# Performance work log

Measured on AMD Instinct MI355X. Metric: run time of the kernel, lower is better.

The kernel has to match this reference:

```python
import jax, jax.numpy as jnp
import numpy as np

N_EMBD = 1024
N_HEAD = 16


def setup_inputs() -> dict:
    key = jax.random.key(0)
    ks = jax.random.split(key, 5)
    B, T, C = 2, 2048, N_EMBD
    x = jax.random.normal(ks[0], (B, T, C), dtype=jnp.float32)
    # parameters (stored as (in, out); forward uses x @ W + b, equivalent to torch Linear)
    s1 = 1.0 / np.sqrt(C)
    W_attn = jax.random.normal(ks[1], (C, 3 * C), dtype=jnp.float32) * s1
    b_attn = jnp.zeros((3 * C,), dtype=jnp.float32)
    W_proj = jax.random.normal(ks[2], (C, C), dtype=jnp.float32) * s1
    b_proj = jnp.zeros((C,), dtype=jnp.float32)
    return {"x": x, "W_attn": W_attn, "b_attn": b_attn, "W_proj": W_proj, "b_proj": b_proj}


def reference(x, W_attn, b_attn, W_proj, b_proj):
    B, T, C = x.shape
    H = N_HEAD
    D = C // H  # head dim
    qkv = x @ W_attn + b_attn                       # [B, T, 3C]
    q, k, v = jnp.split(qkv, 3, axis=-1)
    # [B, H, T, D]
    q = q.reshape(B, T, H, D).transpose(0, 2, 1, 3)
    k = k.reshape(B, T, H, D).transpose(0, 2, 1, 3)
    v = v.reshape(B, T, H, D).transpose(0, 2, 1, 3)
    scale = 1.0 / jnp.sqrt(jnp.asarray(D, dtype=q.dtype))
    wei = jnp.einsum("bhqd,bhkd->bhqk", q, k) * scale  # [B, H, T, T]
    causal = jnp.tril(jnp.ones((T, T), dtype=bool))
    wei = jnp.where(causal[None, None, :, :], wei, -jnp.inf)
    wei = jax.nn.softmax(wei, axis=-1)
    y = jnp.einsum("bhqk,bhkd->bhqd", wei, v)          # [B, H, T, D]
    y = y.transpose(0, 2, 1, 3).reshape(B, T, C)
    return y @ W_proj + b_proj
```

## Files before the change

### kernel.cpp

```cpp
#include <hip/hip_runtime.h>
#include <hip/hip_bf16.h>

typedef __attribute__((ext_vector_type(8))) short short8;
typedef __attribute__((ext_vector_type(4))) float floatx4;
typedef __attribute__((ext_vector_type(4))) unsigned int uintx4;
#define BF16 __hip_bfloat16

__device__ __forceinline__ unsigned short f2bf(float f) {
  unsigned int u = __builtin_bit_cast(unsigned int, f);
  unsigned int r = (u + 0x7FFFu + ((u >> 16) & 1u)) >> 16;
  return (unsigned short)r;
}

__device__ __forceinline__ unsigned int cvt_pk_bf16(float lo, float hi) {
  unsigned int r;
  asm("v_cvt_pk_bf16_f32 %0, %1, %2" : "=v"(r) : "v"(lo), "v"(hi));
  return r;
}

__device__ __forceinline__ void gload_lds16(const void* g, void* l) {
  __builtin_amdgcn_global_load_lds(
      (const __attribute__((address_space(1))) unsigned int*)g,
      (__attribute__((address_space(3))) unsigned int*)l, 16, 0, 0);
}

__global__ __launch_bounds__(256)
void cvt_bf16(const float* __restrict__ in, unsigned short* __restrict__ out, int n) {
  int i = (blockIdx.x * 256 + threadIdx.x) * 8;
  if (i >= n) return;
  float4 a = *(const float4*)(in + i);
  float4 b = *(const float4*)(in + i + 4);
  short8 v;
  v[0] = (short)f2bf(a.x); v[1] = (short)f2bf(a.y);
  v[2] = (short)f2bf(a.z); v[3] = (short)f2bf(a.w);
  v[4] = (short)f2bf(b.x); v[5] = (short)f2bf(b.y);
  v[6] = (short)f2bf(b.z); v[7] = (short)f2bf(b.w);
  *(short8*)(out + i) = v;
}

__global__ __launch_bounds__(256)
void transpose_cvt(const float* __restrict__ in, unsigned short* __restrict__ out,
                   int K, int N) {
  __shared__ float tile[64][65];
  const int nb = N >> 6;
  const int tn = blockIdx.x % nb, tk = blockIdx.x / nb;
  const int n0 = tn << 6, k0 = tk << 6;
  const int tid = threadIdx.x;
#pragma unroll
  for (int c = 0; c < 4; ++c) {
    int t = tid + c * 256;
    int r = t >> 4, col = (t & 15) << 2;
    float4 v = *(const float4*)(in + (size_t)(k0 + r) * N + n0 + col);
    tile[r][col] = v.x; tile[r][col + 1] = v.y;
    tile[r][col + 2] = v.z; tile[r][col + 3] = v.w;
  }
  __syncthreads();
#pragma unroll
  for (int c = 0; c < 2; ++c) {
    int t = tid + c * 256;
    int r = t >> 3, col = (t & 7) << 3;
    short8 v;
#pragma unroll
    for (int j = 0; j < 8; ++j) v[j] = (short)f2bf(tile[col + j][r]);
    *(short8*)(out + (size_t)(n0 + r) * K + k0 + col) = v;
  }
}

template <int EPI>
__global__ __launch_bounds__(256, 2)
void gemm_bt(const BF16* __restrict__ A, const BF16* __restrict__ Bt,
             const float* __restrict__ bias, void* __restrict__ outv,
             int M, int N, int K) {
  const int tid = threadIdx.x;
  const int w = tid >> 6, l = tid & 63;
  const int lr = l & 15, lg = l >> 4;
  const int nbx = N >> 7;
  const int bm = blockIdx.x / nbx, bn = blockIdx.x % nbx;
  const int row0 = bm << 7, col0 = bn << 7;
  const int wr = (w >> 1) << 6, wc = (w & 1) << 6;

  __shared__ __align__(16) BF16 ldsA[128 * 64];
  __shared__ __align__(16) BF16 ldsB[128 * 64];

  floatx4 acc[4][4] = {};
  const int swzl = (lr & 7) << 3;

  for (int k0 = 0; k0 < K; k0 += 64) {
#pragma unroll
    for (int c = 0; c < 4; ++c) {
      int t = w * 64 + l + c * 256;
      int ar = t >> 3;
      int ch = (t & 7) ^ (ar & 7);
      gload_lds16(A + (size_t)(row0 + ar) * K + k0 + (ch << 3),
                  ldsA + w * 512 + c * 2048);
      gload_lds16(Bt + (size_t)(col0 + ar) * K + k0 + (ch << 3),
                  ldsB + w * 512 + c * 2048);
    }
    __syncthreads();
#pragma unroll
    for (int kk = 0; kk < 64; kk += 32) {
      short8 af[4], bf[4];
#pragma unroll
      for (int m = 0; m < 4; ++m)
        af[m] = *(const short8*)(ldsA + (wr + m * 16 + lr) * 64 + ((kk + lg * 8) ^ swzl));
#pragma unroll
      for (int n = 0; n < 4; ++n)
        bf[n] = *(const short8*)(ldsB + (wc + n * 16 + lr) * 64 + ((kk + lg * 8) ^ swzl));
#pragma unroll
      for (int m = 0; m < 4; ++m)
#pragma unroll
        for (int n = 0; n < 4; ++n)
          acc[m][n] = __builtin_amdgcn_mfma_f32_16x16x32_bf16(af[m], bf[n], acc[m][n], 0, 0, 0);
    }
    __syncthreads();
  }

#pragma unroll
  for (int m = 0; m < 4; ++m)
#pragma unroll
    for (int n = 0; n < 4; ++n)
#pragma unroll
      for (int j = 0; j < 4; ++j) {
        int row = row0 + wr + m * 16 + lg * 4 + j;
        int col = col0 + wc + n * 16 + lr;
        float v = acc[m][n][j] + bias[col];
        if (EPI == 0) {
          BF16* out = (BF16*)outv;
          int s = col >> 10, cc = col & 1023;
          int hh = cc >> 6, dd = cc & 63;
          int bb = row >> 11, tt = row & 2047;
          size_t addr;
          if (s == 2)
            addr = (size_t)8388608 + (((size_t)bb * 16 + hh) * 64 + dd) * 2048 + tt;
          else
            addr = (size_t)s * 4194304 + (((size_t)bb * 16 + hh) * 2048 + tt) * 64 + dd;
          out[addr] = __float2bfloat16(v);
        } else {
          float* out = (float*)outv;
          out[(size_t)row * N + col] = v;
        }
      }
}

__global__ __launch_bounds__(256, 4)
void flash_attn(const BF16* __restrict__ qkv, BF16* __restrict__ y) {
  const int T = 2048;
  const int i = blockIdx.x;
  const int xcd = i & 7, s = i >> 3;
  const int par = (s ^ (s >> 5)) & 1;
  const int rnk = ((s >> 5) << 4) | ((s & 31) >> 1);
  const int bh = xcd * 4 + (rnk & 3);
  const int hq = rnk >> 2;
  const int qt = par ? hq : (31 - hq);
  const int b = bh >> 4, h = bh & 15;
  const int q0 = qt << 6;
  const int tid = threadIdx.x, w = tid >> 6, l = tid & 63;
  const int lr = l & 15, lg = l >> 4;

  const BF16* Q  = qkv + (size_t)bh * T * 64;
  const BF16* Kp = qkv + 4194304 + (size_t)bh * T * 64;
  const BF16* Vt = qkv + 8388608 + (size_t)bh * 64 * T;

  __shared__ __align__(16) BF16 ldsK[2][4096];
  __shared__ __align__(16) BF16 ldsV[2][6144];

  const float C1 = 0.18033688011112042f;
  const float C2 = 17.312340490667562f;
  const int swzl = (lr & 7) << 3;
  const int nt = qt + 1;

  short8 qf[2];
#pragma unroll
  for (int c = 0; c < 2; ++c)
    qf[c] = *(const short8*)(Q + (size_t)(q0 + w * 16 + lr) * 64 + c * 32 + lg * 8);

  floatx4 acc_o[4] = {};
  floatx4 lsum4 = {0.f, 0.f, 0.f, 0.f};

  const int t0 = w * 64 + l, t1 = t0 + 256;
  const int r0 = t0 >> 3, ch0 = (t0 & 7) ^ (r0 & 7);
  const int r1 = t1 >> 3, ch1 = (t1 & 7) ^ (r1 & 7);
  const BF16* kg0 = Kp + ((size_t)r0 << 6) + ch0 * 8;
  const BF16* kg1 = Kp + ((size_t)r1 << 6) + ch1 * 8;
  const BF16* vg0 = Vt + (size_t)r0 * T + ch0 * 8;
  const BF16* vg1 = Vt + (size_t)r1 * T + ch1 * 8;

#define STAGE2(BUF)                                           \
  {                                                           \
    gload_lds16(kg0, &ldsK[BUF][w * 512]);                    \
    gload_lds16(vg0, &ldsV[BUF][w * 512]);                    \
    gload_lds16(kg1, &ldsK[BUF][w * 512 + 2048]);             \
    gload_lds16(vg1, &ldsV[BUF][w * 512 + 2048]);             \
    kg0 += 4096; kg1 += 4096; vg0 += 64; vg1 += 64;           \
  }

#define TILE(IT, MASKED)                                                      \
  {                                                                           \
    const int cur_ = (IT) & 1;                                                \
    if ((IT) + 1 < nt) {                                                      \
      STAGE2(cur_ ^ 1);                                                       \
      asm volatile("s_waitcnt vmcnt(4)" ::: "memory");    \
    } else {                                                                  \
      asm volatile("s_waitcnt vmcnt(0)" ::: "memory");                        \
    }                                                                         \
    __builtin_amdgcn_s_barrier();                                             \
                   \
    floatx4 accs[4] = {};                                                     \
    __builtin_amdgcn_s_setprio(1);                                            \
    _Pragma("unroll")                                                         \
    for (int c = 0; c < 2; ++c)                                               \
      _Pragma("unroll")                                                       \
      for (int n4 = 0; n4 < 4; ++n4) {                                        \
        short8 kf = *(const short8*)(&ldsK[cur_][(n4 * 16 + lr) * 64 +        \
                                                ((c * 32 + lg * 8) ^ swzl)]); \
        accs[n4] = __builtin_amdgcn_mfma_f32_16x16x32_bf16(kf, qf[c], accs[n4], 0, 0, 0); \
      }                                                                       \
    __builtin_amdgcn_s_setprio(0);                                            \
                                          \
    _Pragma("unroll")                                                         \
    for (int n4 = 0; n4 < 4; ++n4)                                            \
      _Pragma("unroll")                                                       \
      for (int j = 0; j < 4; ++j) {                                           \
        float p = exp2f(fmaf(accs[n4][j], C1, -C2));                          \
        if (MASKED && (n4 * 16 + lg * 4 + j > w * 16 + lr)) p = 0.f;          \
        lsum4[j] += p;                                                        \
        accs[n4][j] = p;                                                      \
      }                                                                       \
          \
    __builtin_amdgcn_s_setprio(1);                                            \
    _Pragma("unroll")                                                         \
    for (int c = 0; c < 2; ++c) {                                             \
      unsigned int a0 = cvt_pk_bf16(accs[2 * c][0], accs[2 * c][1]);          \
      unsigned int b0 = cvt_pk_bf16(accs[2 * c + 1][0], accs[2 * c + 1][1]);  \
      unsigned int a1 = cvt_pk_bf16(accs[2 * c][2], accs[2 * c][3]);          \
      unsigned int b1 = cvt_pk_bf16(accs[2 * c + 1][2], accs[2 * c + 1][3]);  \
      asm("v_permlane32_swap_b32 %0, %1" : "+v"(a0), "+v"(b0));               \
      asm("v_permlane32_swap_b32 %0, %1" : "+v"(a1), "+v"(b1));               \
      asm("v_permlane16_swap_b32 %0, %1" : "+v"(a0), "+v"(b0));               \
      asm("v_permlane16_swap_b32 %0, %1" : "+v"(a1), "+v"(b1));               \
      uintx4 pw; pw[0] = a0; pw[1] = a1; pw[2] = b0; pw[3] = b1;              \
      short8 pf = __builtin_bit_cast(short8, pw);                             \
      _Pragma("unroll")                                                       \
      for (int n4 = 0; n4 < 4; ++n4) {                                        \
        short8 vf = *(const short8*)(&ldsV[cur_][(n4 * 16 + lr) * 64 +        \
                                                ((c * 32 + lg * 8) ^ swzl)]); \
        acc_o[n4] = __builtin_amdgcn_mfma_f32_16x16x32_bf16(pf, vf, acc_o[n4], 0, 0, 0); \
      }                                                                       \
    }                                                                         \
    __builtin_amdgcn_s_setprio(0);                                            \
    __builtin_amdgcn_s_barrier();                                             \
  }

  STAGE2(0);
  for (int it = 0; it < nt - 1; ++it) TILE(it, false);
  TILE(nt - 1, true);
#undef TILE
#undef STAGE2

  float lsum = (lsum4[0] + lsum4[1]) + (lsum4[2] + lsum4[3]);
  lsum += __shfl_xor(lsum, 16, 64);
  lsum += __shfl_xor(lsum, 32, 64);
  float inv_own = 1.0f / lsum;
  float inv[4];
#pragma unroll
  for (int j = 0; j < 4; ++j) inv[j] = __shfl(inv_own, lg * 4 + j, 64);
#pragma unroll
  for (int n4 = 0; n4 < 4; ++n4)
#pragma unroll
    for (int j = 0; j < 4; ++j) {
      int qr = q0 + w * 16 + lg * 4 + j;
      int dd = n4 * 16 + lr;
      y[((size_t)b * 2048 + qr) * 1024 + h * 64 + dd] =
          __float2bfloat16(acc_o[n4][j] * inv[j]);
    }
}

extern "C" void kernel_launch(void* const* d_in, const int* in_sizes, int n_in,
                              void* d_out, int out_size, void* d_ws, size_t ws_size,
                              hipStream_t stream) {
  const float* x      = (const float*)d_in[0];
  const float* W_attn = (const float*)d_in[1];
  const float* b_attn = (const float*)d_in[2];
  const float* W_proj = (const float*)d_in[3];
  const float* b_proj = (const float*)d_in[4];
  float* out = (float*)d_out;
  BF16* ws  = (BF16*)d_ws;

  BF16* xb      = ws;
  BF16* wt_attn = xb + 4194304;
  BF16* wt_proj = wt_attn + 3145728;
  BF16* qkv     = wt_proj + 1048576;
  BF16* y       = qkv + 12582912;

  hipLaunchKernelGGL(cvt_bf16, dim3(2048), dim3(256), 0, stream,
                     x, (unsigned short*)xb, 4194304);
  hipLaunchKernelGGL(transpose_cvt, dim3(48 * 16), dim3(256), 0, stream,
                     W_attn, (unsigned short*)wt_attn, 1024, 3072);
  hipLaunchKernelGGL(transpose_cvt, dim3(16 * 16), dim3(256), 0, stream,
                     W_proj, (unsigned short*)wt_proj, 1024, 1024);
  hipLaunchKernelGGL(gemm_bt<0>, dim3(32 * 24), dim3(256), 0, stream,
                     xb, wt_attn, b_attn, (void*)qkv, 4096, 3072, 1024);
  hipLaunchKernelGGL(flash_attn, dim3(1024), dim3(256), 0, stream, qkv, y);
  hipLaunchKernelGGL(gemm_bt<1>, dim3(32 * 8), dim3(256), 0, stream,
                     y, wt_proj, b_proj, (void*)out, 4096, 1024, 1024);
}
```

Baseline: 109.6 us.

## Triple-buffer QKV GEMM with async global-to-LDS loads and BK=32

Replaces the QKV projection GEMM with a dedicated kernel that uses a three-stage LDS ring of 32-wide K tiles. Tiles are filled by direct global-to-LDS loads issued two iterations ahead, with vmcnt waits and raw barriers. The swizzle is adapted to the narrower tiles and occupancy is raised to three blocks per CU. The goal is to overlap global-load latency with MFMA work instead of the previous synchronous staging, at the cost of more barriers per unit of K work. The output projection keeps the old kernel with its epilogue specialized.

```diff
diff --git a/kernel.cpp b/kernel.cpp
--- a/kernel.cpp
+++ b/kernel.cpp
@@ -66,11 +66,101 @@
   }
 }
 
-template <int EPI>
+__global__ __launch_bounds__(256, 3)
+void gemm_qkv3(const BF16* __restrict__ A, const BF16* __restrict__ Bt,
+               const float* __restrict__ bias, BF16* __restrict__ out,
+               int M, int N, int K) {
+  const int tid = threadIdx.x;
+  const int w = tid >> 6, l = tid & 63;
+  const int lr = l & 15, lg = l >> 4;
+  const int nbx = N >> 7;
+  const int bm = blockIdx.x / nbx, bn = blockIdx.x % nbx;
+  const int row0 = bm << 7, col0 = bn << 7;
+  const int wr = (w >> 1) << 6, wc = (w & 1) << 6;
+
+  __shared__ __align__(16) BF16 ldsA[3][128 * 32];
+  __shared__ __align__(16) BF16 ldsB[3][128 * 32];
+
+  floatx4 acc[4][4] = {};
+  const int swzl = ((lr >> 1) & 3) << 3;
+
+#define STAGE(K0, BUF)                                                        \
+  { _Pragma("unroll")                                                         \
+    for (int c = 0; c < 2; ++c) {                                             \
+      int t_ = w * 64 + l + c * 256;                  \
+      int r_ = t_ >> 2;                                                       \
+      int ch_ = (t_ & 3) ^ ((r_ >> 1) & 3);                                   \
+      gload_lds16(A + (size_t)(row0 + r_) * K + (K0) + (ch_ << 3),            \
+                  &ldsA[BUF][w * 512 + c * 2048]);                            \
+      gload_lds16(Bt + (size_t)(col0 + r_) * K + (K0) + (ch_ << 3),           \
+                  &ldsB[BUF][w * 512 + c * 2048]);                            \
+    } }
+
+#define FBARRIER asm volatile("s_barrier" ::: "memory")
+
+  const int NT = K >> 5;
+  STAGE(0, 0);
+  asm volatile("" ::: "memory");
+  STAGE(32, 1);
+  asm volatile("" ::: "memory");
+  int cur = 0, nx2 = 2;
+
+  for (int t = 0; t < NT; ++t) {
+    if (t + 2 < NT) {
+      STAGE((t + 2) << 5, nx2);
+      asm volatile("s_waitcnt vmcnt(8)" ::: "memory");
+    } else if (t + 1 < NT) {
+      asm volatile("s_waitcnt vmcnt(4)" ::: "memory");
+    } else {
+      asm volatile("s_waitcnt vmcnt(0)" ::: "memory");
+    }
+    FBARRIER;
+
+    short8 af[4], bf[4];
+#pragma unroll
+    for (int m = 0; m < 4; ++m)
+      af[m] = *(const short8*)(&ldsA[cur][(wr + m * 16 + lr) * 32 + ((lg * 8) ^ swzl)]);
+#pragma unroll
+    for (int n = 0; n < 4; ++n)
+      bf[n] = *(const short8*)(&ldsB[cur][(wc + n * 16 + lr) * 32 + ((lg * 8) ^ swzl)]);
+#pragma unroll
+    for (int m = 0; m < 4; ++m)
+#pragma unroll
+      for (int n = 0; n < 4; ++n)
+        acc[m][n] = __builtin_amdgcn_mfma_f32_16x16x32_bf16(af[m], bf[n], acc[m][n], 0, 0, 0);
+
+    FBARRIER;
+    cur = (cur == 2) ? 0 : cur + 1;
+    nx2 = (nx2 == 2) ? 0 : nx2 + 1;
+  }
+#undef STAGE
+#undef FBARRIER
+
+#pragma unroll
+  for (int m = 0; m < 4; ++m)
+#pragma unroll
+    for (int n = 0; n < 4; ++n)
+#pragma unroll
+      for (int j = 0; j < 4; ++j) {
+        int row = row0 + wr + m * 16 + lg * 4 + j;
+        int col = col0 + wc + n * 16 + lr;
+        float v = acc[m][n][j] + bias[col];
+        int s = col >> 10, cc = col & 1023;
+        int hh = cc >> 6, dd = cc & 63;
+        int bb = row >> 11, tt = row & 2047;
+        size_t addr;
+        if (s == 2)
+          addr = (size_t)8388608 + (((size_t)bb * 16 + hh) * 64 + dd) * 2048 + tt;
+        else
+          addr = (size_t)s * 4194304 + (((size_t)bb * 16 + hh) * 2048 + tt) * 64 + dd;
+        out[addr] = __float2bfloat16(v);
+      }
+}
+
 __global__ __launch_bounds__(256, 2)
-void gemm_bt(const BF16* __restrict__ A, const BF16* __restrict__ Bt,
-             const float* __restrict__ bias, void* __restrict__ outv,
-             int M, int N, int K) {
+void gemm_proj(const BF16* __restrict__ A, const BF16* __restrict__ Bt,
+               const float* __restrict__ bias, float* __restrict__ out,
+               int M, int N, int K) {
   const int tid = threadIdx.x;
   const int w = tid >> 6, l = tid & 63;
   const int lr = l & 15, lg = l >> 4;
@@ -123,22 +213,7 @@
       for (int j = 0; j < 4; ++j) {
         int row = row0 + wr + m * 16 + lg * 4 + j;
         int col = col0 + wc + n * 16 + lr;
-        float v = acc[m][n][j] + bias[col];
-        if (EPI == 0) {
-          BF16* out = (BF16*)outv;
-          int s = col >> 10, cc = col & 1023;
-          int hh = cc >> 6, dd = cc & 63;
-          int bb = row >> 11, tt = row & 2047;
-          size_t addr;
-          if (s == 2)
-            addr = (size_t)8388608 + (((size_t)bb * 16 + hh) * 64 + dd) * 2048 + tt;
-          else
-            addr = (size_t)s * 4194304 + (((size_t)bb * 16 + hh) * 2048 + tt) * 64 + dd;
-          out[addr] = __float2bfloat16(v);
-        } else {
-          float* out = (float*)outv;
-          out[(size_t)row * N + col] = v;
-        }
+        out[(size_t)row * N + col] = acc[m][n][j] + bias[col];
       }
 }
 
@@ -204,7 +279,6 @@
       asm volatile("s_waitcnt vmcnt(0)" ::: "memory");                        \
     }                                                                         \
     __builtin_amdgcn_s_barrier();                                             \
-                   \
     floatx4 accs[4] = {};                                                     \
     __builtin_amdgcn_s_setprio(1);                                            \
     _Pragma("unroll")                                                         \
@@ -216,7 +290,6 @@
         accs[n4] = __builtin_amdgcn_mfma_f32_16x16x32_bf16(kf, qf[c], accs[n4], 0, 0, 0); \
       }                                                                       \
     __builtin_amdgcn_s_setprio(0);                                            \
-                                          \
     _Pragma("unroll")                                                         \
     for (int n4 = 0; n4 < 4; ++n4)                                            \
       _Pragma("unroll")                                                       \
@@ -226,7 +299,6 @@
         lsum4[j] += p;                                                        \
         accs[n4][j] = p;                                                      \
       }                                                                       \
-          \
     __builtin_amdgcn_s_setprio(1);                                            \
     _Pragma("unroll")                                                         \
     for (int c = 0; c < 2; ++c) {                                             \
@@ -298,9 +370,9 @@
                      W_attn, (unsigned short*)wt_attn, 1024, 3072);
   hipLaunchKernelGGL(transpose_cvt, dim3(16 * 16), dim3(256), 0, stream,
                      W_proj, (unsigned short*)wt_proj, 1024, 1024);
-  hipLaunchKernelGGL(gemm_bt<0>, dim3(32 * 24), dim3(256), 0, stream,
-                     xb, wt_attn, b_attn, (void*)qkv, 4096, 3072, 1024);
+  hipLaunchKernelGGL(gemm_qkv3, dim3(32 * 24), dim3(256), 0, stream,
+                     xb, wt_attn, b_attn, qkv, 4096, 3072, 1024);
   hipLaunchKernelGGL(flash_attn, dim3(1024), dim3(256), 0, stream, qkv, y);
-  hipLaunchKernelGGL(gemm_bt<1>, dim3(32 * 8), dim3(256), 0, stream,
-                     y, wt_proj, b_proj, (void*)out, 4096, 1024, 1024);
-}
+  hipLaunchKernelGGL(gemm_proj, dim3(32 * 8), dim3(256), 0, stream,
+                     y, wt_proj, b_proj, out, 4096, 1024, 1024);
+}
```

Result: slower. 115.8 us (+5.7%).

## Fuse prep kernels, retile projection GEMM, shrink attention V LDS buffer

Applied to the files above, without the earlier changes.

Merges the x conversion and both weight transpose-conversions into one launch, cutting two kernel launches. Replaces the projection GEMM with a 64x128 tile variant that launches 512 blocks instead of 256 at higher occupancy, so the grid fills more CUs. Shrinks the flash-attention V LDS buffer from 6144 to 4096 elements per stage and raises launch bounds to 5 blocks per CU for more occupancy. The risk is register pressure under the tighter bound, and any padding the larger V buffer provided is gone.

```diff
diff --git a/kernel.cpp b/kernel.cpp
--- a/kernel.cpp
+++ b/kernel.cpp
@@ -25,27 +25,34 @@
 }
 
 __global__ __launch_bounds__(256)
-void cvt_bf16(const float* __restrict__ in, unsigned short* __restrict__ out, int n) {
-  int i = (blockIdx.x * 256 + threadIdx.x) * 8;
-  if (i >= n) return;
-  float4 a = *(const float4*)(in + i);
-  float4 b = *(const float4*)(in + i + 4);
-  short8 v;
-  v[0] = (short)f2bf(a.x); v[1] = (short)f2bf(a.y);
-  v[2] = (short)f2bf(a.z); v[3] = (short)f2bf(a.w);
-  v[4] = (short)f2bf(b.x); v[5] = (short)f2bf(b.y);
-  v[6] = (short)f2bf(b.z); v[7] = (short)f2bf(b.w);
-  *(short8*)(out + i) = v;
-}
-
-__global__ __launch_bounds__(256)
-void transpose_cvt(const float* __restrict__ in, unsigned short* __restrict__ out,
-                   int K, int N) {
+void prep_fused(const float* __restrict__ x, unsigned short* __restrict__ xb,
+                const float* __restrict__ Wa, unsigned short* __restrict__ wta,
+                const float* __restrict__ Wp, unsigned short* __restrict__ wtp) {
   __shared__ float tile[64][65];
+  const int blk = blockIdx.x;
+  const int tid = threadIdx.x;
+
+  if (blk < 2048) {
+    int i = (blk * 256 + tid) * 8;
+    float4 a = *(const float4*)(x + i);
+    float4 b = *(const float4*)(x + i + 4);
+    short8 v;
+    v[0] = (short)f2bf(a.x); v[1] = (short)f2bf(a.y);
+    v[2] = (short)f2bf(a.z); v[3] = (short)f2bf(a.w);
+    v[4] = (short)f2bf(b.x); v[5] = (short)f2bf(b.y);
+    v[6] = (short)f2bf(b.z); v[7] = (short)f2bf(b.w);
+    *(short8*)(xb + i) = v;
+    return;
+  }
+
+  const float* in;
+  unsigned short* out;
+  int K = 1024, N, bb;
+  if (blk < 2816) { in = Wa; out = wta; N = 3072; bb = blk - 2048; }
+  else            { in = Wp; out = wtp; N = 1024; bb = blk - 2816; }
   const int nb = N >> 6;
-  const int tn = blockIdx.x % nb, tk = blockIdx.x / nb;
+  const int tn = bb % nb, tk = bb / nb;
   const int n0 = tn << 6, k0 = tk << 6;
-  const int tid = threadIdx.x;
 #pragma unroll
   for (int c = 0; c < 4; ++c) {
     int t = tid + c * 256;
@@ -66,11 +73,10 @@
   }
 }
 
-template <int EPI>
 __global__ __launch_bounds__(256, 2)
-void gemm_bt(const BF16* __restrict__ A, const BF16* __restrict__ Bt,
-             const float* __restrict__ bias, void* __restrict__ outv,
-             int M, int N, int K) {
+void gemm_qkv(const BF16* __restrict__ A, const BF16* __restrict__ Bt,
+              const float* __restrict__ bias, BF16* __restrict__ out,
+              int M, int N, int K) {
   const int tid = threadIdx.x;
   const int w = tid >> 6, l = tid & 63;
   const int lr = l & 15, lg = l >> 4;
@@ -124,25 +130,84 @@
         int row = row0 + wr + m * 16 + lg * 4 + j;
         int col = col0 + wc + n * 16 + lr;
         float v = acc[m][n][j] + bias[col];
-        if (EPI == 0) {
-          BF16* out = (BF16*)outv;
-          int s = col >> 10, cc = col & 1023;
-          int hh = cc >> 6, dd = cc & 63;
-          int bb = row >> 11, tt = row & 2047;
-          size_t addr;
-          if (s == 2)
-            addr = (size_t)8388608 + (((size_t)bb * 16 + hh) * 64 + dd) * 2048 + tt;
-          else
-            addr = (size_t)s * 4194304 + (((size_t)bb * 16 + hh) * 2048 + tt) * 64 + dd;
-          out[addr] = __float2bfloat16(v);
-        } else {
-          float* out = (float*)outv;
-          out[(size_t)row * N + col] = v;
-        }
+        int s = col >> 10, cc = col & 1023;
+        int hh = cc >> 6, dd = cc & 63;
+        int bb = row >> 11, tt = row & 2047;
+        size_t addr;
+        if (s == 2)
+          addr = (size_t)8388608 + (((size_t)bb * 16 + hh) * 64 + dd) * 2048 + tt;
+        else
+          addr = (size_t)s * 4194304 + (((size_t)bb * 16 + hh) * 2048 + tt) * 64 + dd;
+        out[addr] = __float2bfloat16(v);
       }
 }
 
 __global__ __launch_bounds__(256, 4)
+void gemm_proj(const BF16* __restrict__ A, const BF16* __restrict__ Bt,
+               const float* __restrict__ bias, float* __restrict__ out,
+               int M, int N, int K) {
+  const int tid = threadIdx.x;
+  const int w = tid >> 6, l = tid & 63;
+  const int lr = l & 15, lg = l >> 4;
+  const int bm = blockIdx.x >> 3, bn = blockIdx.x & 7;
+  const int row0 = bm << 6, col0 = bn << 7;
+  const int wr = (w >> 1) << 5, wc = (w & 1) << 6;
+
+  __shared__ __align__(16) BF16 ldsA[64 * 64];
+  __shared__ __align__(16) BF16 ldsB[128 * 64];
+
+  floatx4 acc[2][4] = {};
+  const int swzl = (lr & 7) << 3;
+
+  for (int k0 = 0; k0 < K; k0 += 64) {
+#pragma unroll
+    for (int c = 0; c < 2; ++c) {
+      int t = w * 64 + l + c * 256;
+      int ar = t >> 3;
+      int ch = (t & 7) ^ (ar & 7);
+      gload_lds16(A + (size_t)(row0 + ar) * K + k0 + (ch << 3),
+                  ldsA + w * 512 + c * 2048);
+    }
+#pragma unroll
+    for (int c = 0; c < 4; ++c) {
+      int t = w * 64 + l + c * 256;
+      int br = t >> 3;
+      int ch = (t & 7) ^ (br & 7);
+      gload_lds16(Bt + (size_t)(col0 + br) * K + k0 + (ch << 3),
+                  ldsB + w * 512 + c * 2048);
+    }
+    __syncthreads();
+#pragma unroll
+    for (int kk = 0; kk < 64; kk += 32) {
+      short8 af[2], bf[4];
+#pragma unroll
+      for (int m = 0; m < 2; ++m)
+        af[m] = *(const short8*)(ldsA + (wr + m * 16 + lr) * 64 + ((kk + lg * 8) ^ swzl));
+#pragma unroll
+      for (int n = 0; n < 4; ++n)
+        bf[n] = *(const short8*)(ldsB + (wc + n * 16 + lr) * 64 + ((kk + lg * 8) ^ swzl));
+#pragma unroll
+      for (int m = 0; m < 2; ++m)
+#pragma unroll
+        for (int n = 0; n < 4; ++n)
+          acc[m][n] = __builtin_amdgcn_mfma_f32_16x16x32_bf16(af[m], bf[n], acc[m][n], 0, 0, 0);
+    }
+    __syncthreads();
+  }
+
+#pragma unroll
+  for (int m = 0; m < 2; ++m)
+#pragma unroll
+    for (int n = 0; n < 4; ++n)
+#pragma unroll
+      for (int j = 0; j < 4; ++j) {
+        int row = row0 + wr + m * 16 + lg * 4 + j;
+        int col = col0 + wc + n * 16 + lr;
+        out[(size_t)row * N + col] = acc[m][n][j] + bias[col];
+      }
+}
+
+__global__ __launch_bounds__(256, 5)
 void flash_attn(const BF16* __restrict__ qkv, BF16* __restrict__ y) {
   const int T = 2048;
   const int i = blockIdx.x;
@@ -162,7 +227,7 @@
   const BF16* Vt = qkv + 8388608 + (size_t)bh * 64 * T;
 
   __shared__ __align__(16) BF16 ldsK[2][4096];
-  __shared__ __align__(16) BF16 ldsV[2][6144];
+  __shared__ __align__(16) BF16 ldsV[2][4096];
 
   const float C1 = 0.18033688011112042f;
   const float C2 = 17.312340490667562f;
@@ -204,7 +269,6 @@
       asm volatile("s_waitcnt vmcnt(0)" ::: "memory");                        \
     }                                                                         \
     __builtin_amdgcn_s_barrier();                                             \
-                   \
     floatx4 accs[4] = {};                                                     \
     __builtin_amdgcn_s_setprio(1);                                            \
     _Pragma("unroll")                                                         \
@@ -216,7 +280,6 @@
         accs[n4] = __builtin_amdgcn_mfma_f32_16x16x32_bf16(kf, qf[c], accs[n4], 0, 0, 0); \
       }                                                                       \
     __builtin_amdgcn_s_setprio(0);                                            \
-                                          \
     _Pragma("unroll")                                                         \
     for (int n4 = 0; n4 < 4; ++n4)                                            \
       _Pragma("unroll")                                                       \
@@ -226,7 +289,6 @@
         lsum4[j] += p;                                                        \
         accs[n4][j] = p;                                                      \
       }                                                                       \
-          \
     __builtin_amdgcn_s_setprio(1);                                            \
     _Pragma("unroll")                                                         \
     for (int c = 0; c < 2; ++c) {                                             \
@@ -292,15 +354,13 @@
   BF16* qkv     = wt_proj + 1048576;
   BF16* y       = qkv + 12582912;
 
-  hipLaunchKernelGGL(cvt_bf16, dim3(2048), dim3(256), 0, stream,
-                     x, (unsigned short*)xb, 4194304);
-  hipLaunchKernelGGL(transpose_cvt, dim3(48 * 16), dim3(256), 0, stream,
-                     W_attn, (unsigned short*)wt_attn, 1024, 3072);
-  hipLaunchKernelGGL(transpose_cvt, dim3(16 * 16), dim3(256), 0, stream,
-                     W_proj, (unsigned short*)wt_proj, 1024, 1024);
-  hipLaunchKernelGGL(gemm_bt<0>, dim3(32 * 24), dim3(256), 0, stream,
-                     xb, wt_attn, b_attn, (void*)qkv, 4096, 3072, 1024);
+  hipLaunchKernelGGL(prep_fused, dim3(3072), dim3(256), 0, stream,
+                     x, (unsigned short*)xb,
+                     W_attn, (unsigned short*)wt_attn,
+                     W_proj, (unsigned short*)wt_proj);
+  hipLaunchKernelGGL(gemm_qkv, dim3(32 * 24), dim3(256), 0, stream,
+                     xb, wt_attn, b_attn, qkv, 4096, 3072, 1024);
   hipLaunchKernelGGL(flash_attn, dim3(1024), dim3(256), 0, stream, qkv, y);
-  hipLaunchKernelGGL(gemm_bt<1>, dim3(32 * 8), dim3(256), 0, stream,
-                     y, wt_proj, b_proj, (void*)out, 4096, 1024, 1024);
-}
+  hipLaunchKernelGGL(gemm_proj, dim3(512), dim3(256), 0, stream,
+                     y, wt_proj, b_proj, out, 4096, 1024, 1024);
+}
```

Measured after the change: 103.1 us (median of 2 runs). 1.06x faster.
